# Kernel optimization log

Measured on AMD Instinct MI355X. Metric: run time of the kernel, lower is better.

The kernel has to match this reference:

```python
import jax, jax.numpy as jnp
import numpy as np

DT = 0.1
EPS = 0.01


def _trans_layer(x, W, b):
    # x: [B, 2U]; W: [U, U]; b: [U]
    U = b.shape[0]
    t = DT / EPS
    u_in, v_in = x[:, :U], x[:, U:]
    act = jnp.tanh(u_in)
    v_star = (v_in + t * act) / (1.0 + t)
    # Block matrix A = [[I, dt*W], [-dt*W^T, I]] -- identical for all samples,
    # so factor/solve ONCE with a multi-RHS solve instead of torch's per-sample batched LU.
    I = jnp.eye(U, dtype=x.dtype)
    A = jnp.block([[I, DT * W], [-DT * W.T, I]])  # [2U, 2U]
    rhs = jnp.concatenate([u_in + DT * b, v_star], axis=1)  # [B, 2U]
    y = jnp.linalg.solve(A, rhs.T).T  # [B, 2U]
    u, v = y[:, :U], y[:, U:]
    u_out = DT * (v @ W.T) - u_in - DT * b
    v_out = -DT * (u @ W) + t * v - v_in - t * act
    return jnp.concatenate([u_out, v_out], axis=1)


def setup_inputs() -> dict:
    key = jax.random.key(0)
    ks = jax.random.split(key, 14)
    B, D_IN, U, D_OUT = 32768, 256, 256, 10

    def lin_w(k, o, i):
        return (jax.random.uniform(k, (o, i), jnp.float32) * 2.0 - 1.0) / np.sqrt(i).astype(np.float32)

    def lin_b(k, o, fan_in):
        return (jax.random.uniform(k, (o,), jnp.float32) * 2.0 - 1.0) / np.sqrt(fan_in).astype(np.float32)

    return {
        'x': jax.random.normal(ks[0], (B, D_IN), jnp.float32),
        'Wi': lin_w(ks[1], U, D_IN), 'bi': lin_b(ks[2], U, D_IN),
        'W1': lin_w(ks[3], U, U), 'b1': lin_b(ks[4], U, U),
        'W2': lin_w(ks[5], U, U), 'b2': lin_b(ks[6], U, U),
        'W3': lin_w(ks[7], U, U), 'b3': lin_b(ks[8], U, U),
        'W4': lin_w(ks[9], U, U), 'b4': lin_b(ks[10], U, U),
        'Wo': lin_w(ks[11], D_OUT, U), 'bo': lin_b(ks[12], D_OUT, U),
    }


def reference(x, Wi, bi, W1, b1, W2, b2, W3, b3, W4, b4, Wo, bo):
    U = W1.shape[0]
    z = x @ Wi.T + bi                       # linearInput
    z = jnp.concatenate([z, jnp.tanh(z)], axis=1)  # [B, 2U]
    for W, b in ((W1, b1), (W2, b2), (W3, b3), (W4, b4)):
        z = _trans_layer(z, W, b)
    z = z[:, :U]
    logits = z @ Wo.T + bo                  # linearOutput
    return jax.nn.softmax(logits, axis=1)
```

## Files before the change

### kernel.cpp

```cpp
#include <hip/hip_runtime.h>
#include <math.h>

#define DTC 0.1f

typedef _Float16 half8 __attribute__((ext_vector_type(8)));
typedef _Float16 half4v __attribute__((ext_vector_type(4)));
typedef float f32x4 __attribute__((ext_vector_type(4)));
typedef float f32x2 __attribute__((ext_vector_type(2)));

__device__ __forceinline__ float fast_tanh(float x) {
  const float e = __expf(2.f * x);
  const float r = __builtin_amdgcn_rcpf(e + 1.f);
  return fmaf(-2.f, r, 1.f);
}


__global__ __launch_bounds__(256) void k_prep(
    const float* __restrict__ W0, const float* __restrict__ W1,
    const float* __restrict__ W2, const float* __restrict__ W3,
    const float* __restrict__ b2, const float* __restrict__ b3,
    const float* __restrict__ b4,
    _Float16* __restrict__ Wh, _Float16* __restrict__ Wt,
    float* __restrict__ crm) {
  const float* Ws[4] = {W0, W1, W2, W3};
  const int bid = blockIdx.x, tid = threadIdx.x;
  if (bid < 128) {
    const int t = bid * 256 + tid;
    const float* W = Ws[(t * 8) >> 16];
    const int off = (t * 8) & 65535;
    const float4 a = *(const float4*)&W[off];
    const float4 b = *(const float4*)&W[off + 4];
    half8 h;
    h[0] = (_Float16)a.x; h[1] = (_Float16)a.y; h[2] = (_Float16)a.z; h[3] = (_Float16)a.w;
    h[4] = (_Float16)b.x; h[5] = (_Float16)b.y; h[6] = (_Float16)b.z; h[7] = (_Float16)b.w;
    *(half8*)&Wh[t * 8] = h;
  } else if (bid < 384) {
    __shared__ float sh[32][33];
    const int b2i = bid - 128;
    const int l = b2i >> 6, t64 = b2i & 63;
    const int r0 = (t64 >> 3) * 32, c0 = (t64 & 7) * 32;
    const float* W = Ws[l];
    const int i = tid >> 5, j = tid & 31;
#pragma unroll
    for (int p = 0; p < 4; ++p)
      sh[p * 8 + i][j] = W[(r0 + p * 8 + i) * 256 + c0 + j];
    __syncthreads();
#pragma unroll
    for (int p = 0; p < 4; ++p)
      Wt[l * 65536 + (c0 + p * 8 + i) * 256 + r0 + j] = (_Float16)sh[j][p * 8 + i];
  } else {
    const int l = bid - 384;
    const float* W = Ws[l];
    const float* b = (l == 0) ? b2 : (l == 1) ? b3 : b4;
    float s = 0.f;
#pragma unroll 8
    for (int k = 0; k < 256; ++k) s = fmaf(b[k], W[k * 256 + tid], s);
    crm[l * 256 + tid] = -0.09f * s;
  }
}

__global__ __launch_bounds__(256) void k_smm3(const _Float16* __restrict__ A,
                                              const _Float16* __restrict__ B,
                                              const _Float16* __restrict__ Eadd,
                                              _Float16* __restrict__ C,
                                              float scale, int addI) {
  const int tid = threadIdx.x, wave = tid >> 6, lane = tid & 63;
  const int quad = lane >> 4, l16 = lane & 15;
  const int l = blockIdx.z;
  const _Float16* Al = A + (size_t)l * 65536;
  const _Float16* Bl = B + (size_t)l * 65536;
  _Float16* Cl = C + (size_t)l * 65536;
  const int m0 = blockIdx.y * 64 + wave * 16, n0 = blockIdx.x * 64;
  f32x4 acc[4] = {};
#pragma unroll
  for (int kt = 0; kt < 8; ++kt) {
    const half8 af = *(const half8*)&Al[(m0 + l16) * 256 + kt * 32 + quad * 8];
#pragma unroll
    for (int ni = 0; ni < 4; ++ni) {
      const half8 bf = *(const half8*)&Bl[(n0 + ni * 16 + l16) * 256 + kt * 32 + quad * 8];
      acc[ni] = __builtin_amdgcn_mfma_f32_16x16x32_f16(af, bf, acc[ni], 0, 0, 0);
    }
  }
#pragma unroll
  for (int ni = 0; ni < 4; ++ni)
#pragma unroll
    for (int r = 0; r < 4; ++r) {
      const int row = m0 + quad * 4 + r, col = n0 + ni * 16 + l16;
      float v = scale * acc[ni][r];
      if (addI) v += (row == col ? 1.f : 0.f) - (float)(Eadd + (size_t)l * 65536)[row * 256 + col];
      Cl[row * 256 + col] = (_Float16)v;
    }
}

__global__ __launch_bounds__(256) void k_pack(
    const _Float16* __restrict__ Ph, const _Float16* __restrict__ Qt,
    const _Float16* __restrict__ Wt, const float* __restrict__ Wi,
    const float* __restrict__ Wo,
    _Float16* __restrict__ PQP, _Float16* __restrict__ RmP,
    _Float16* __restrict__ WiP, _Float16* __restrict__ WoP) {
  const int t = blockIdx.x * 256 + threadIdx.x;
  if (t < 65536) {
    const int l = t >> 14, c = t & 16383;
    const int ntile = c >> 10, kt = (c >> 6) & 15, lb = c & 63;
    const int n = ntile * 16 + (lb & 15);
    const int kq = (lb >> 4) * 8;
    half8 h;
    if (kt < 8) {
      h = *(const half8*)&Ph[(size_t)l * 65536 + n * 256 + kt * 32 + kq];
#pragma unroll
      for (int j = 0; j < 8; ++j) h[j] = -h[j];
    } else {
      h = *(const half8*)&Qt[(size_t)l * 65536 + n * 256 + (kt - 8) * 32 + kq];
    }
    *(half8*)&PQP[(size_t)t * 8] = h;
  } else if (t < 90112) {
    const int tt = t - 65536;
    const int l = tt >> 13, c = tt & 8191;
    const int ntile = c >> 9, kt = (c >> 6) & 7, lb = c & 63;
    const int n = ntile * 16 + (lb & 15);
    const int k0 = kt * 32 + (lb >> 4) * 8;
    half8 h = *(const half8*)&Wt[(size_t)l * 65536 + n * 256 + k0];
#pragma unroll
    for (int j = 0; j < 8; ++j) h[j] = (_Float16)(-0.9f * (float)h[j]);
    *(half8*)&RmP[(size_t)tt * 8] = h;
  } else if (t < 98304) {
    const int c = t - 90112;
    const int ntile = c >> 9, kt = (c >> 6) & 7, lb = c & 63;
    const int n = ntile * 16 + (lb & 15);
    const int k0 = kt * 32 + (lb >> 4) * 8;
    const float4 a = *(const float4*)&Wi[n * 256 + k0];
    const float4 b = *(const float4*)&Wi[n * 256 + k0 + 4];
    half8 h;
    h[0] = (_Float16)a.x; h[1] = (_Float16)a.y; h[2] = (_Float16)a.z; h[3] = (_Float16)a.w;
    h[4] = (_Float16)b.x; h[5] = (_Float16)b.y; h[6] = (_Float16)b.z; h[7] = (_Float16)b.w;
    *(half8*)&WiP[(size_t)c * 8] = h;
  } else {
    const int c = t - 98304;
    const int kt = c >> 6, lb = c & 63;
    const int n = lb & 15;
    const int k0 = kt * 32 + (lb >> 4) * 8;
    half8 h;
#pragma unroll
    for (int j = 0; j < 8; ++j) h[j] = (_Float16)((n < 10) ? Wo[n * 256 + k0 + j] : 0.f);
    *(half8*)&WoP[(size_t)c * 8] = h;
  }
}



template <int NKT, bool DUAL>
__device__ __forceinline__ void gemm_k(const _Float16* __restrict__ Bp,
                                       const _Float16* A1, const _Float16* A2,
                                       f32x4* acc, int wave, int lane) {
  half8 bf[4][4];
  auto loadB = [&](int kt, int s) {
#pragma unroll
    for (int ni = 0; ni < 4; ++ni)
      bf[s][ni] = *(const half8*)&Bp[(((wave * 4 + ni) * NKT + kt) * 64 + lane) * 8];
  };
  loadB(0, 0);
  loadB(1, 1);
  loadB(2, 2);
  const char* a1b = (const char*)A1 + lane * 16;
  const char* a2b = (const char*)A2 + lane * 16;
#pragma unroll
  for (int kt = 0; kt < NKT; ++kt) {
    const int s = kt & 3;
    if (kt + 3 < NKT) loadB(kt + 3, (kt + 3) & 3);
    const char* Ab = (DUAL && kt >= NKT / 2) ? a2b : a1b;
    const int akt = DUAL ? (kt & (NKT / 2 - 1)) : kt;
    half8 af[4];
#pragma unroll
    for (int mi = 0; mi < 4; ++mi)
      af[mi] = *(const half8*)(Ab + (akt * 4 + mi) * 1024);
    __builtin_amdgcn_s_setprio(1);
#pragma unroll
    for (int mi = 0; mi < 4; ++mi)
#pragma unroll
      for (int ni = 0; ni < 4; ++ni)
        acc[mi * 4 + ni] = __builtin_amdgcn_mfma_f32_16x16x32_f16(
            bf[s][ni], af[mi], acc[mi * 4 + ni], 0, 0, 0);
    __builtin_amdgcn_s_setprio(0);
  }
}

__global__ __launch_bounds__(256, 2) void k_fused(
    const float* __restrict__ x, const _Float16* __restrict__ WiP,
    const _Float16* __restrict__ PQP, const _Float16* __restrict__ RmP,
    const _Float16* __restrict__ WoP, const float* __restrict__ bi,
    const float* __restrict__ b1, const float* __restrict__ b2,
    const float* __restrict__ b3, const float* __restrict__ b4,
    const float* __restrict__ crm, const float* __restrict__ bo,
    float* __restrict__ out) {
  __shared__ __align__(16) _Float16 A1[64 * 256];
  __shared__ __align__(16) _Float16 A2[64 * 256];
  const int tid = threadIdx.x;
  const int wave = tid >> 6, lane = tid & 63;
  const int quad = lane >> 4, l16 = lane & 15;
  const int m0 = blockIdx.x * 64;

#pragma unroll
  for (int kk = 0; kk < 2; ++kk) {
    const int kt = wave + kk * 4;
#pragma unroll
    for (int mi = 0; mi < 4; ++mi) {
      const size_t gb = (size_t)(m0 + mi * 16 + l16) * 256 + kt * 32 + quad * 8;
      const float4 a = *(const float4*)&x[gb];
      const float4 b = *(const float4*)&x[gb + 4];
      half8 h;
      h[0] = (_Float16)a.x; h[1] = (_Float16)a.y; h[2] = (_Float16)a.z; h[3] = (_Float16)a.w;
      h[4] = (_Float16)b.x; h[5] = (_Float16)b.y; h[6] = (_Float16)b.z; h[7] = (_Float16)b.w;
      *(half8*)((char*)A1 + ((kt * 4 + mi) * 64 + lane) * 16) = h;
    }
  }
  __syncthreads();

  f32x4 acc[16];
  const f32x4 zero = {0.f, 0.f, 0.f, 0.f};
  half4v uph[16];

  const int ebase = wave * 8192 + (quad >> 1) * 256 + l16 * 16 + (quad & 1) * 8;
  char* e1 = (char*)A1 + ebase;
  char* e2 = (char*)A2 + ebase;

#pragma unroll
  for (int t = 0; t < 16; ++t) acc[t] = zero;
  gemm_k<8, false>(WiP, A1, A1, acc, wave, lane);
  __syncthreads();
#pragma unroll
  for (int ni = 0; ni < 4; ++ni) {
    const int col0 = wave * 64 + ni * 16 + quad * 4;
    const f32x4 bi4 = *(const f32x4*)&bi[col0];
    const f32x4 b14 = *(const f32x4*)&b1[col0];
#pragma unroll
    for (int mi = 0; mi < 4; ++mi) {
      const int off = (ni >> 1) * 4096 + mi * 1024 + (ni & 1) * 512;
      half4v h1, h2;
#pragma unroll
      for (int r = 0; r < 4; ++r) {
        const float z = acc[mi * 4 + ni][r] + bi4[r];
        h1[r] = (_Float16)(z + DTC * b14[r]);
        h2[r] = (_Float16)fast_tanh(z);
      }
      *(half4v*)(e1 + off) = h1;
      *(half4v*)(e2 + off) = h2;
    }
  }
  __syncthreads();

#pragma unroll 1
  for (int l = 0; l < 4; ++l) {
#pragma unroll
    for (int t = 0; t < 16; ++t) acc[t] = zero;
    gemm_k<16, true>(PQP + (size_t)l * 131072, A1, A2, acc, wave, lane);
    __syncthreads();
    const float* bn = (l == 0) ? b2 : (l == 1) ? b3 : b4;
#pragma unroll
    for (int ni = 0; ni < 4; ++ni) {
      const int col0 = wave * 64 + ni * 16 + quad * 4;
      f32x4 bn4 = zero;
      if (l < 3) bn4 = DTC * (*(const f32x4*)&bn[col0]);
#pragma unroll
      for (int mi = 0; mi < 4; ++mi) {
        const int off = (ni >> 1) * 4096 + mi * 1024 + (ni & 1) * 512;
        half4v hu, h1;
#pragma unroll
        for (int r = 0; r < 4; ++r) {
          const float u = acc[mi * 4 + ni][r];
          hu[r] = (_Float16)u;
          h1[r] = (_Float16)(u + bn4[r]);
        }
        uph[mi * 4 + ni] = hu;
        *(half4v*)(e1 + off) = h1;
      }
    }
    __syncthreads();
    if (l < 3) {
#pragma unroll
      for (int t = 0; t < 16; ++t) acc[t] = zero;
      gemm_k<8, false>(RmP + (size_t)l * 65536, A1, A1, acc, wave, lane);
#pragma unroll
      for (int ni = 0; ni < 4; ++ni) {
        const int col0 = wave * 64 + ni * 16 + quad * 4;
        const f32x4 cc4 = *(const f32x4*)&crm[l * 256 + col0];
#pragma unroll
        for (int mi = 0; mi < 4; ++mi) {
          const int off = (ni >> 1) * 4096 + mi * 1024 + (ni & 1) * 512;
          const half4v r2o = *(const half4v*)(e2 + off);
          half4v nr2;
#pragma unroll
          for (int r = 0; r < 4; ++r) {
            const float vp = acc[mi * 4 + ni][r] - cc4[r] - (float)r2o[r];
            nr2[r] = (_Float16)((vp + 10.f * fast_tanh((float)uph[mi * 4 + ni][r])) * (1.f / 11.f));
          }
          *(half4v*)(e2 + off) = nr2;
        }
      }
      __syncthreads();
    }
  }

  {
    f32x4 acch = zero;
#pragma unroll
    for (int kt = 0; kt < 8; ++kt) {
      const half8 af = *(const half8*)((const char*)A1 +
                                       ((kt * 4 + wave) * 64 + lane) * 16);
      const half8 bfr = *(const half8*)&WoP[(kt * 64 + lane) * 8];
      acch = __builtin_amdgcn_mfma_f32_16x16x32_f16(bfr, af, acch, 0, 0, 0);
    }
    float v4[4];
    float mx = -3.0e38f;
#pragma unroll
    for (int r = 0; r < 4; ++r) {
      const int cls = quad * 4 + r;
      const float v = acch[r] + ((cls < 10) ? bo[cls] : -3.0e38f);
      v4[r] = v;
      mx = fmaxf(mx, v);
    }
    mx = fmaxf(mx, __shfl_xor(mx, 16, 64));
    mx = fmaxf(mx, __shfl_xor(mx, 32, 64));
    float e4[4], s = 0.f;
#pragma unroll
    for (int r = 0; r < 4; ++r) {
      e4[r] = __expf(v4[r] - mx);
      s += e4[r];
    }
    s += __shfl_xor(s, 16, 64);
    s += __shfl_xor(s, 32, 64);
    const float rs = __builtin_amdgcn_rcpf(s);
    float* op = &out[(size_t)(m0 + wave * 16 + l16) * 10 + quad * 4];
    if (quad < 2) {
      f32x2 p0 = {e4[0] * rs, e4[1] * rs};
      f32x2 p1 = {e4[2] * rs, e4[3] * rs};
      *(f32x2*)op = p0;
      *(f32x2*)(op + 2) = p1;
    } else if (quad == 2) {
      f32x2 p0 = {e4[0] * rs, e4[1] * rs};
      *(f32x2*)op = p0;
    }
  }
}


extern "C" void kernel_launch(void* const* d_in, const int* in_sizes, int n_in,
                              void* d_out, int out_size, void* d_ws, size_t ws_size,
                              hipStream_t stream) {
  const float* x  = (const float*)d_in[0];
  const float* Wi = (const float*)d_in[1];
  const float* bi = (const float*)d_in[2];
  const float* W[4] = {(const float*)d_in[3], (const float*)d_in[5],
                       (const float*)d_in[7], (const float*)d_in[9]};
  const float* b[4] = {(const float*)d_in[4], (const float*)d_in[6],
                       (const float*)d_in[8], (const float*)d_in[10]};
  const float* Wo = (const float*)d_in[11];
  const float* bo = (const float*)d_in[12];
  float* out = (float*)d_out;

  const int Bsz = in_sizes[0] / 256;

  _Float16* hb = (_Float16*)d_ws;
  _Float16* WiP = hb;
  _Float16* WoP = hb + 65536;
  _Float16* PQP = hb + 69632;
  _Float16* RmP = hb + 593920;
  _Float16* Wh  = hb + 790528;
  _Float16* Wt  = hb + 1052672;
  _Float16* Eh  = hb + 1314816;
  _Float16* Ph  = hb + 1576960;
  _Float16* Qt  = hb + 1839104;
  float* crm = (float*)(hb + 2101248);

  const dim3 g64(4, 4, 4);
  k_prep<<<387, 256, 0, stream>>>(W[0], W[1], W[2], W[3], b[1], b[2], b[3],
                                  Wh, Wt, crm);
  k_smm3<<<g64, 256, 0, stream>>>(Wh, Wh, nullptr, Eh, 0.01f, 0);
  k_smm3<<<g64, 256, 0, stream>>>(Eh, Eh, Eh, Ph, 1.0f, 1);
  k_smm3<<<g64, 256, 0, stream>>>(Ph, Wt, nullptr, Qt, DTC, 0);
  k_pack<<<386, 256, 0, stream>>>(Ph, Qt, Wt, Wi, Wo, PQP, RmP, WiP, WoP);

  k_fused<<<Bsz / 64, 256, 0, stream>>>(x, WiP, PQP, RmP, WoP, bi,
                                        b[0], b[1], b[2], b[3], crm, bo, out);
}
```

Baseline: 183.0 us.

## Prefetch next GEMM's B fragments across epilogues and use LDS-only barriers

Hoists the first three B-fragment loads of each GEMM out of gemm_k into a shared register ring. Each next GEMM's weights are now prefetched before the preceding barrier and epilogue, so global load latency overlaps epilogue work. It also replaces __syncthreads with a barrier that waits only on LDS counters (lgkmcnt), so in-flight global loads no longer stall the barrier. Bias and crm loads are hoisted ahead of the barrier as well. The cost is more live registers at the barriers, which could cause spills or reduce occupancy under launch_bounds(256,2).

```diff
diff --git a/kernel.cpp b/kernel.cpp
--- a/kernel.cpp
+++ b/kernel.cpp
@@ -12,6 +12,11 @@
   const float e = __expf(2.f * x);
   const float r = __builtin_amdgcn_rcpf(e + 1.f);
   return fmaf(-2.f, r, 1.f);
+}
+
+__device__ __forceinline__ void bar_lds() {
+  asm volatile("s_waitcnt lgkmcnt(0)" ::: "memory");
+  __builtin_amdgcn_s_barrier();
 }
 
 
@@ -148,25 +153,32 @@
 
 
 
+template <int NKT>
+__device__ __forceinline__ void preB(const _Float16* __restrict__ Bp,
+                                     half8 bf[4][4], int wave, int lane) {
+#pragma unroll
+  for (int s = 0; s < 3; ++s)
+#pragma unroll
+    for (int ni = 0; ni < 4; ++ni)
+      bf[s][ni] = *(const half8*)&Bp[(((wave * 4 + ni) * NKT + s) * 64 + lane) * 8];
+}
+
 template <int NKT, bool DUAL>
 __device__ __forceinline__ void gemm_k(const _Float16* __restrict__ Bp,
                                        const _Float16* A1, const _Float16* A2,
-                                       f32x4* acc, int wave, int lane) {
-  half8 bf[4][4];
-  auto loadB = [&](int kt, int s) {
-#pragma unroll
-    for (int ni = 0; ni < 4; ++ni)
-      bf[s][ni] = *(const half8*)&Bp[(((wave * 4 + ni) * NKT + kt) * 64 + lane) * 8];
-  };
-  loadB(0, 0);
-  loadB(1, 1);
-  loadB(2, 2);
+                                       f32x4* acc, half8 bf[4][4],
+                                       int wave, int lane) {
   const char* a1b = (const char*)A1 + lane * 16;
   const char* a2b = (const char*)A2 + lane * 16;
 #pragma unroll
   for (int kt = 0; kt < NKT; ++kt) {
     const int s = kt & 3;
-    if (kt + 3 < NKT) loadB(kt + 3, (kt + 3) & 3);
+    if (kt + 3 < NKT) {
+#pragma unroll
+      for (int ni = 0; ni < 4; ++ni)
+        bf[(kt + 3) & 3][ni] =
+            *(const half8*)&Bp[(((wave * 4 + ni) * NKT + kt + 3) * 64 + lane) * 8];
+    }
     const char* Ab = (DUAL && kt >= NKT / 2) ? a2b : a1b;
     const int akt = DUAL ? (kt & (NKT / 2 - 1)) : kt;
     half8 af[4];
@@ -213,11 +225,14 @@
       *(half8*)((char*)A1 + ((kt * 4 + mi) * 64 + lane) * 16) = h;
     }
   }
-  __syncthreads();
 
   f32x4 acc[16];
   const f32x4 zero = {0.f, 0.f, 0.f, 0.f};
   half4v uph[16];
+  half8 ring[4][4];
+
+  preB<8>(WiP, ring, wave, lane);
+  bar_lds();
 
   const int ebase = wave * 8192 + (quad >> 1) * 256 + l16 * 16 + (quad & 1) * 8;
   char* e1 = (char*)A1 + ebase;
@@ -225,41 +240,50 @@
 
 #pragma unroll
   for (int t = 0; t < 16; ++t) acc[t] = zero;
-  gemm_k<8, false>(WiP, A1, A1, acc, wave, lane);
-  __syncthreads();
+  gemm_k<8, false>(WiP, A1, A1, acc, ring, wave, lane);
+  f32x4 bi4[4], b14[4];
 #pragma unroll
   for (int ni = 0; ni < 4; ++ni) {
     const int col0 = wave * 64 + ni * 16 + quad * 4;
-    const f32x4 bi4 = *(const f32x4*)&bi[col0];
-    const f32x4 b14 = *(const f32x4*)&b1[col0];
+    bi4[ni] = *(const f32x4*)&bi[col0];
+    b14[ni] = *(const f32x4*)&b1[col0];
+  }
+  preB<16>(PQP, ring, wave, lane);
+  bar_lds();
+#pragma unroll
+  for (int ni = 0; ni < 4; ++ni) {
 #pragma unroll
     for (int mi = 0; mi < 4; ++mi) {
       const int off = (ni >> 1) * 4096 + mi * 1024 + (ni & 1) * 512;
       half4v h1, h2;
 #pragma unroll
       for (int r = 0; r < 4; ++r) {
-        const float z = acc[mi * 4 + ni][r] + bi4[r];
-        h1[r] = (_Float16)(z + DTC * b14[r]);
+        const float z = acc[mi * 4 + ni][r] + bi4[ni][r];
+        h1[r] = (_Float16)(z + DTC * b14[ni][r]);
         h2[r] = (_Float16)fast_tanh(z);
       }
       *(half4v*)(e1 + off) = h1;
       *(half4v*)(e2 + off) = h2;
     }
   }
-  __syncthreads();
+  bar_lds();
 
 #pragma unroll 1
   for (int l = 0; l < 4; ++l) {
 #pragma unroll
     for (int t = 0; t < 16; ++t) acc[t] = zero;
-    gemm_k<16, true>(PQP + (size_t)l * 131072, A1, A2, acc, wave, lane);
-    __syncthreads();
+    gemm_k<16, true>(PQP + (size_t)l * 131072, A1, A2, acc, ring, wave, lane);
     const float* bn = (l == 0) ? b2 : (l == 1) ? b3 : b4;
+    f32x4 bn4[4];
 #pragma unroll
     for (int ni = 0; ni < 4; ++ni) {
-      const int col0 = wave * 64 + ni * 16 + quad * 4;
-      f32x4 bn4 = zero;
-      if (l < 3) bn4 = DTC * (*(const f32x4*)&bn[col0]);
+      bn4[ni] = zero;
+      if (l < 3) bn4[ni] = DTC * (*(const f32x4*)&bn[wave * 64 + ni * 16 + quad * 4]);
+    }
+    if (l < 3) preB<8>(RmP + (size_t)l * 65536, ring, wave, lane);
+    bar_lds();
+#pragma unroll
+    for (int ni = 0; ni < 4; ++ni) {
 #pragma unroll
       for (int mi = 0; mi < 4; ++mi) {
         const int off = (ni >> 1) * 4096 + mi * 1024 + (ni & 1) * 512;
@@ -268,21 +292,24 @@
         for (int r = 0; r < 4; ++r) {
           const float u = acc[mi * 4 + ni][r];
           hu[r] = (_Float16)u;
-          h1[r] = (_Float16)(u + bn4[r]);
+          h1[r] = (_Float16)(u + bn4[ni][r]);
         }
         uph[mi * 4 + ni] = hu;
         *(half4v*)(e1 + off) = h1;
       }
     }
-    __syncthreads();
+    bar_lds();
     if (l < 3) {
 #pragma unroll
       for (int t = 0; t < 16; ++t) acc[t] = zero;
-      gemm_k<8, false>(RmP + (size_t)l * 65536, A1, A1, acc, wave, lane);
+      gemm_k<8, false>(RmP + (size_t)l * 65536, A1, A1, acc, ring, wave, lane);
+      f32x4 cc4[4];
+#pragma unroll
+      for (int ni = 0; ni < 4; ++ni)
+        cc4[ni] = *(const f32x4*)&crm[l * 256 + wave * 64 + ni * 16 + quad * 4];
+      preB<16>(PQP + (size_t)(l + 1) * 131072, ring, wave, lane);
 #pragma unroll
       for (int ni = 0; ni < 4; ++ni) {
-        const int col0 = wave * 64 + ni * 16 + quad * 4;
-        const f32x4 cc4 = *(const f32x4*)&crm[l * 256 + col0];
 #pragma unroll
         for (int mi = 0; mi < 4; ++mi) {
           const int off = (ni >> 1) * 4096 + mi * 1024 + (ni & 1) * 512;
@@ -290,13 +317,13 @@
           half4v nr2;
 #pragma unroll
           for (int r = 0; r < 4; ++r) {
-            const float vp = acc[mi * 4 + ni][r] - cc4[r] - (float)r2o[r];
+            const float vp = acc[mi * 4 + ni][r] - cc4[ni][r] - (float)r2o[r];
             nr2[r] = (_Float16)((vp + 10.f * fast_tanh((float)uph[mi * 4 + ni][r])) * (1.f / 11.f));
           }
           *(half4v*)(e2 + off) = nr2;
         }
       }
-      __syncthreads();
+      bar_lds();
     }
   }
 
```

Result: slower. 210.0 us (+14.8%).
